# Optimization experiments

Measured on AMD Instinct MI355X. Metric: run time of the kernel, lower is better.

Reference implementation:

```python
import jax, jax.numpy as jnp
import numpy as np

WS = 16            # window size (patch grid)
NP = WS * WS       # 256 patch tokens
N = NP + 1         # +1 CLS
H = 16             # heads
LN_EPS = 1e-5


def _rel_pos_index():
    ch, cw = np.meshgrid(np.arange(WS), np.arange(WS), indexing='ij')
    flat = np.stack([ch.reshape(-1), cw.reshape(-1)])            # [2, NP]
    rel = flat[:, :, None] - flat[:, None, :]                    # [2, NP, NP]
    rel = rel.transpose(1, 2, 0).astype(np.int64)                # [NP, NP, 2]
    rel[:, :, 0] += WS - 1
    rel[:, :, 1] += WS - 1
    rel[:, :, 0] *= 2 * WS - 1
    nrd = (2 * WS - 1) * (2 * WS - 1) + 3                        # 964
    idx = np.zeros((N, N), dtype=np.int64)
    idx[1:, 1:] = rel.sum(-1)
    idx[0, 0:] = nrd - 3
    idx[0:, 0] = nrd - 2
    idx[0, 0] = nrd - 1
    return idx

REL_IDX = _rel_pos_index()


def layernorm(x, g, b):
    mu = x.mean(-1, keepdims=True)
    var = x.var(-1, keepdims=True)
    return (x - mu) * jax.lax.rsqrt(var + LN_EPS) * g + b


def rotate_half(t):
    t1, t2 = t[..., ::2], t[..., 1::2]
    return jnp.stack([-t2, t1], axis=-1).reshape(t.shape)


def apply_rope(t, cos, sin):
    # t: [B, H, NP, hd]; cos/sin: [NP, hd]
    return t * cos + rotate_half(t) * sin


def setup_inputs() -> dict:
    key = jax.random.key(0)
    ks = jax.random.split(key, 20)
    D, Hd = 1024, 4096
    s = lambda d: 1.0 / np.sqrt(d)
    return {
        'x': jax.random.normal(ks[0], (64, N, D), jnp.float32),
        'rope_cos': jnp.cos(jnp.arange(NP)[:, None] * jnp.exp(-jnp.arange(64) / 16.0)[None, :]),
        'rope_sin': jnp.sin(jnp.arange(NP)[:, None] * jnp.exp(-jnp.arange(64) / 16.0)[None, :]),
        'q_w': jax.random.normal(ks[1], (D, D)) * s(D),
        'q_b': jnp.zeros((D,)),
        'k_w': jax.random.normal(ks[2], (D, D)) * s(D),
        'v_w': jax.random.normal(ks[3], (D, D)) * s(D),
        'v_b': jnp.zeros((D,)),
        'rel_bias_table': jax.random.normal(ks[4], (964, H)) * 0.02,
        'inner_ln_g': jnp.ones((D,)), 'inner_ln_b': jnp.zeros((D,)),
        'proj_w': jax.random.normal(ks[5], (D, D)) * s(D),
        'proj_b': jnp.zeros((D,)),
        'norm1_g': jnp.ones((D,)), 'norm1_b': jnp.zeros((D,)),
        'norm2_g': jnp.ones((D,)), 'norm2_b': jnp.zeros((D,)),
        'w1_w': jax.random.normal(ks[6], (Hd, D)) * s(D),
        'w1_b': jnp.zeros((Hd,)),
        'w2_w': jax.random.normal(ks[7], (Hd, D)) * s(D),
        'w2_b': jnp.zeros((Hd,)),
        'ffn_ln_g': jnp.ones((Hd,)), 'ffn_ln_b': jnp.zeros((Hd,)),
        'w3_w': jax.random.normal(ks[8], (D, Hd)) * s(Hd),
        'w3_b': jnp.zeros((D,)),
    }


def reference(x, rope_cos, rope_sin, q_w, q_b, k_w, v_w, v_b, rel_bias_table,
              inner_ln_g, inner_ln_b, proj_w, proj_b, norm1_g, norm1_b,
              norm2_g, norm2_b, w1_w, w1_b, w2_w, w2_b, ffn_ln_g, ffn_ln_b,
              w3_w, w3_b):
    B, Ntok, D = x.shape
    hd = D // H
    scale = hd ** -0.5

    # ---- attention branch (pre-norm, subln path) ----
    xn = layernorm(x, norm1_g, norm1_b)
    q = (xn @ q_w.T + q_b).reshape(B, Ntok, H, hd).transpose(0, 2, 1, 3)
    k = (xn @ k_w.T).reshape(B, Ntok, H, hd).transpose(0, 2, 1, 3)
    v = (xn @ v_w.T + v_b).reshape(B, Ntok, H, hd).transpose(0, 2, 1, 3)

    # RoPE on all tokens except CLS
    q = jnp.concatenate([q[:, :, :1], apply_rope(q[:, :, 1:], rope_cos, rope_sin)], axis=2)
    k = jnp.concatenate([k[:, :, :1], apply_rope(k[:, :, 1:], rope_cos, rope_sin)], axis=2)

    attn = jnp.einsum('bhqd,bhkd->bhqk', q * scale, k)
    # relative position bias: [N, N, H] -> [H, N, N]
    rel_bias = rel_bias_table[REL_IDX.reshape(-1)].reshape(Ntok, Ntok, H).transpose(2, 0, 1)
    attn = attn + rel_bias[None]
    attn = jax.nn.softmax(attn, axis=-1)

    out = jnp.einsum('bhqk,bhkd->bqhd', attn, v).reshape(B, Ntok, D)
    out = layernorm(out, inner_ln_g, inner_ln_b)     # inner_attn_ln (subln)
    out = out @ proj_w.T + proj_b
    x = x + out

    # ---- SwiGLU MLP branch ----
    xn2 = layernorm(x, norm2_g, norm2_b)
    x1 = xn2 @ w1_w.T + w1_b
    x2 = xn2 @ w2_w.T + w2_b
    hidden = jax.nn.silu(x1) * x2
    hidden = layernorm(hidden, ffn_ln_g, ffn_ln_b)   # ffn_ln (subln)
    x = x + (hidden @ w3_w.T + w3_b)
    return x
```

## Files before the change

### kernel.cpp

```cpp
#include <hip/hip_runtime.h>
#include <stdint.h>

typedef __bf16 bf16;
typedef __attribute__((ext_vector_type(8))) __bf16 bf16x8;
typedef __attribute__((ext_vector_type(4))) float floatx4;

__device__ inline float bflo(uint32_t u){ union{uint32_t v; float f;} t; t.v = u << 16; return t.f; }
__device__ inline float bfhi(uint32_t u){ union{uint32_t v; float f;} t; t.v = u & 0xffff0000u; return t.f; }
__device__ inline uint32_t pack2(float a, float b){ union{ bf16 h[2]; uint32_t u; } t; t.h[0]=(bf16)a; t.h[1]=(bf16)b; return t.u; }

__device__ inline void load4(const bf16* p, float* x){
  uint2 u = *(const uint2*)p; x[0]=bflo(u.x); x[1]=bfhi(u.x); x[2]=bflo(u.y); x[3]=bfhi(u.y);
}
__device__ inline void load4(const float* p, float* x){
  float4 u = *(const float4*)p; x[0]=u.x; x[1]=u.y; x[2]=u.z; x[3]=u.w;
}

__device__ inline void gload16(const void* g, void* l){
  __builtin_amdgcn_global_load_lds((const __attribute__((address_space(1))) uint32_t*)g,
                                   (__attribute__((address_space(3))) uint32_t*)l, 16, 0, 0);
}

__global__ __launch_bounds__(256) void cvt_kernel(const float* __restrict__ in, bf16* __restrict__ out, int n8)
{
  int i = blockIdx.x * 256 + threadIdx.x;
  if (i >= n8) return;
  const float* p = in + (size_t)i * 8;
  float4 a = *(const float4*)p;
  float4 b = *(const float4*)(p + 4);
  union{ uint4 q; bf16 h[8]; } pk;
  pk.h[0]=(bf16)a.x; pk.h[1]=(bf16)a.y; pk.h[2]=(bf16)a.z; pk.h[3]=(bf16)a.w;
  pk.h[4]=(bf16)b.x; pk.h[5]=(bf16)b.y; pk.h[6]=(bf16)b.z; pk.h[7]=(bf16)b.w;
  *(uint4*)(out + (size_t)i*8) = pk.q;
}

template<int W, typename TIN>
__global__ __launch_bounds__(256) void ln_kernel(const TIN* in, const float* __restrict__ g,
                                                 const float* __restrict__ bb, bf16* out, int M)
{
  constexpr int E = W / 256;
  int row = blockIdx.x; if (row >= M) return;
  int tid = threadIdx.x;
  const TIN* rp = in + (size_t)row * W + tid * E;
  float x[E];
  #pragma unroll
  for (int j = 0; j < E; j += 4) load4(rp + j, &x[j]);
  float s = 0.f, ss = 0.f;
  #pragma unroll
  for (int e = 0; e < E; e++){ s += x[e]; ss += x[e]*x[e]; }
  #pragma unroll
  for (int k = 32; k >= 1; k >>= 1){ s += __shfl_xor(s, k, 64); ss += __shfl_xor(ss, k, 64); }
  __shared__ float rs_[4], rq_[4];
  if ((tid & 63) == 0){ rs_[tid >> 6] = s; rq_[tid >> 6] = ss; }
  __syncthreads();
  s = rs_[0]+rs_[1]+rs_[2]+rs_[3]; ss = rq_[0]+rq_[1]+rq_[2]+rq_[3];
  float mean = s * (1.0f / W);
  float var  = ss * (1.0f / W) - mean * mean;
  float rinv = rsqrtf(var + 1e-5f);
  bf16* op = out + (size_t)row * W + tid * E;
  const float* gp = g + tid * E;
  const float* bp = bb + tid * E;
  #pragma unroll
  for (int j = 0; j < E; j += 4){
    float gv[4], bv[4];
    load4(gp + j, gv); load4(bp + j, bv);
    float y0 = (x[j]  -mean)*rinv*gv[0] + bv[0];
    float y1 = (x[j+1]-mean)*rinv*gv[1] + bv[1];
    float y2 = (x[j+2]-mean)*rinv*gv[2] + bv[2];
    float y3 = (x[j+3]-mean)*rinv*gv[3] + bv[3];
    uint2 o; o.x = pack2(y0, y1); o.y = pack2(y2, y3);
    *(uint2*)(op + j) = o;
  }
}

template<typename TE, typename TC>
__global__ __launch_bounds__(256) void gemm_bt(const bf16* __restrict__ A, const bf16* __restrict__ Bw,
                                               const float* __restrict__ bias, const TE* extra,
                                               TC* C, int M, int N, int K, int mode)
{
  __shared__ __align__(16) bf16 As[128*32];
  __shared__ __align__(16) bf16 Bs[128*32];
  int tid = threadIdx.x;
  int lane = tid & 63, wave = tid >> 6;
  int l16 = lane & 15, quad = lane >> 4;
  int wm = wave >> 1, wn = wave & 1;
  int m0 = blockIdx.y * 128, n0 = blockIdx.x * 128;
  floatx4 acc[4][4];
  #pragma unroll
  for (int i = 0; i < 4; i++)
    #pragma unroll
    for (int j = 0; j < 4; j++) acc[i][j] = (floatx4){0.f,0.f,0.f,0.f};
  int nk = K >> 5;

  int rowS = tid >> 2;
  int colS = (tid & 3) * 8;
  int ra0 = min(m0 + rowS,      M-1);
  int ra1 = min(m0 + 64 + rowS, M-1);
  int rb0 = min(n0 + rowS,      N-1);
  int rb1 = min(n0 + 64 + rowS, N-1);
  const bf16* pa0 = A  + (size_t)ra0 * K + colS;
  const bf16* pa1 = A  + (size_t)ra1 * K + colS;
  const bf16* pb0 = Bw + (size_t)rb0 * K + colS;
  const bf16* pb1 = Bw + (size_t)rb1 * K + colS;
  bf16* la0 = &As[tid*8];        bf16* la1 = &As[2048 + tid*8];
  bf16* lb0 = &Bs[tid*8];        bf16* lb1 = &Bs[2048 + tid*8];
  auto stage = [&](int kt){
    int ko = kt * 32;
    gload16(pa0 + ko, la0);
    gload16(pa1 + ko, la1);
    gload16(pb0 + ko, lb0);
    gload16(pb1 + ko, lb1);
  };

  stage(0);
  int kt = 0;
  while (true){
    __syncthreads();
    bf16x8 af[4], bfv[4];
    #pragma unroll
    for (int i = 0; i < 4; i++) af[i]  = *(const bf16x8*)&As[(wm*64 + i*16 + l16)*32 + quad*8];
    #pragma unroll
    for (int j = 0; j < 4; j++) bfv[j] = *(const bf16x8*)&Bs[(wn*64 + j*16 + l16)*32 + quad*8];
    ++kt;
    bool more = kt < nk;
    if (more){
      __syncthreads();
      stage(kt);
    }
    #pragma unroll
    for (int i = 0; i < 4; i++)
      #pragma unroll
      for (int j = 0; j < 4; j++)
        acc[i][j] = __builtin_amdgcn_mfma_f32_16x16x32_bf16(af[i], bfv[j], acc[i][j], 0, 0, 0);
    if (!more) break;
  }

  #pragma unroll
  for (int i = 0; i < 4; i++){
    int gmb = m0 + wm*64 + i*16 + quad*4;
    #pragma unroll
    for (int j = 0; j < 4; j++){
      int gn = n0 + wn*64 + j*16 + l16;
      float bv = bias ? bias[gn] : 0.f;
      #pragma unroll
      for (int r = 0; r < 4; r++){
        int gm = gmb + r;
        if (gm < M){
          float v = acc[i][j][r] + bv;
          if (mode == 1) v += (float)extra[(size_t)gm * N + gn];
          else if (mode == 2){ float a = (float)extra[(size_t)gm * N + gn]; v *= a / (1.f + __expf(-a)); }
          C[(size_t)gm * N + gn] = (TC)v;
        }
      }
    }
  }
}

__global__ __launch_bounds__(256) void rope_kernel(bf16* __restrict__ q, bf16* __restrict__ k,
                                                   const float* __restrict__ cs, const float* __restrict__ sn)
{
  uint32_t i = blockIdx.x * 256u + threadIdx.x;
  int d0 = (int)(i & 511) * 2;
  int tok = (int)((i >> 9) & 255);
  int b = (int)(i >> 17);
  int j = d0 & 63;
  float c0 = cs[tok*64 + j], c1 = cs[tok*64 + j + 1];
  float s0 = sn[tok*64 + j], s1 = sn[tok*64 + j + 1];
  size_t off = ((size_t)(b*257 + tok + 1)) * 1024 + d0;
  uint32_t uq = *(const uint32_t*)(q + off);
  float x0 = bflo(uq), x1 = bfhi(uq);
  *(uint32_t*)(q + off) = pack2(x0*c0 - x1*s0, x1*c1 + x0*s1);
  uint32_t uk = *(const uint32_t*)(k + off);
  float y0 = bflo(uk), y1 = bfhi(uk);
  *(uint32_t*)(k + off) = pack2(y0*c0 - y1*s0, y1*c1 + y0*s1);
}

__global__ __launch_bounds__(256) void attn_kernel(const bf16* __restrict__ Q, const bf16* __restrict__ Kg,
                                                   const bf16* __restrict__ Vg, const float* __restrict__ tab,
                                                   bf16* __restrict__ AO)
{
  __shared__ __align__(16) bf16 Kc[144*64];
  __shared__ __align__(16) bf16 Vt[64*160];
  __shared__ __align__(16) float S[16*160];
  __shared__ __align__(16) bf16 P[16*160];
  __shared__ float mrow[16], lrow[16], arow[16];
  int id = blockIdx.x;
  int qt = id % 17; int rest = id / 17;
  int h = rest & 15; int b = rest >> 4;
  int tid = threadIdx.x; int wave = tid >> 6; int lane = tid & 63;
  int l16 = lane & 15, quad = lane >> 4;
  size_t base = ((size_t)b * 257) * 1024 + h * 64;
  int q0 = qt * 16;
  int tokA = min(q0 + l16, 256);
  const bf16* qp = Q + base + (size_t)tokA * 1024;
  bf16x8 a0 = *(const bf16x8*)(qp + quad*8);
  bf16x8 a1 = *(const bf16x8*)(qp + 32 + quad*8);
  floatx4 o = (floatx4){0.f,0.f,0.f,0.f};
  if (tid < 16){ mrow[tid] = -1e30f; lrow[tid] = 0.f; }
  for (int ch = 0; ch < 2; ch++){
    int t0 = ch * 144;
    __syncthreads();
    for (int i = tid; i < 144*8; i += 256){
      int row = i >> 3, c8 = (i & 7) * 8;
      int tok = t0 + row;
      uint4 u = make_uint4(0,0,0,0);
      if (tok <= 256) u = *(const uint4*)(Kg + base + (size_t)tok*1024 + c8);
      *(uint4*)&Kc[row*64 + c8] = u;
    }
    for (int i = tid; i < 160*8; i += 256){
      int trow = i >> 3, c8 = (i & 7) * 8;
      int tok = t0 + trow;
      uint4 u = make_uint4(0,0,0,0);
      if (trow < 144 && tok <= 256) u = *(const uint4*)(Vg + base + (size_t)tok*1024 + c8);
      union { uint4 q4; bf16 h8[8]; } tmp; tmp.q4 = u;
      #pragma unroll
      for (int jj = 0; jj < 8; jj++) Vt[(c8 + jj)*160 + trow] = tmp.h8[jj];
    }
    __syncthreads();
    for (int nt = wave; nt < 9; nt += 4){
      int kr = nt*16 + l16;
      bf16x8 b0 = *(const bf16x8*)&Kc[kr*64 + quad*8];
      bf16x8 b1 = *(const bf16x8*)&Kc[kr*64 + 32 + quad*8];
      floatx4 c = (floatx4){0.f,0.f,0.f,0.f};
      c = __builtin_amdgcn_mfma_f32_16x16x32_bf16(a0, b0, c, 0, 0, 0);
      c = __builtin_amdgcn_mfma_f32_16x16x32_bf16(a1, b1, c, 0, 0, 0);
      #pragma unroll
      for (int r = 0; r < 4; r++) S[(quad*4 + r)*160 + nt*16 + l16] = c[r];
    }
    __syncthreads();
    {
      int r = tid >> 4, li = tid & 15;
      int qg = q0 + r; bool vrow = qg <= 256;
      float vals[10]; float mc = -1e30f;
      #pragma unroll
      for (int jj = 0; jj < 10; jj++){
        int c = li + 16*jj; int kg = t0 + c;
        float sv = -1e30f;
        if (vrow && c < 144 && kg <= 256){
          int idx;
          if (qg == 0 && kg == 0) idx = 963;
          else if (qg == 0) idx = 961;
          else if (kg == 0) idx = 962;
          else { int p = qg - 1, pk = kg - 1;
                 idx = ((p >> 4) - (pk >> 4) + 15) * 31 + ((p & 15) - (pk & 15) + 15); }
          sv = S[r*160 + c] * 0.125f + tab[idx*16 + h];
        }
        vals[jj] = sv; mc = fmaxf(mc, sv);
      }
      #pragma unroll
      for (int k = 8; k >= 1; k >>= 1) mc = fmaxf(mc, __shfl_xor(mc, k, 16));
      float mold = mrow[r];
      float mnew = fmaxf(mold, mc);
      float alpha = __expf(mold - mnew);
      float sum = 0.f;
      #pragma unroll
      for (int jj = 0; jj < 10; jj++){
        float p = (vals[jj] > -1e29f) ? __expf(vals[jj] - mnew) : 0.f;
        sum += p;
        P[r*160 + li + 16*jj] = (bf16)p;
      }
      #pragma unroll
      for (int k = 8; k >= 1; k >>= 1) sum += __shfl_xor(sum, k, 16);
      if (li == 0){ mrow[r] = mnew; lrow[r] = lrow[r]*alpha + sum; arow[r] = alpha; }
    }
    __syncthreads();
    #pragma unroll
    for (int r2 = 0; r2 < 4; r2++) o[r2] *= arow[quad*4 + r2];
    #pragma unroll
    for (int ks = 0; ks < 5; ks++){
      bf16x8 pa = *(const bf16x8*)&P[l16*160 + ks*32 + quad*8];
      bf16x8 vb = *(const bf16x8*)&Vt[(wave*16 + l16)*160 + ks*32 + quad*8];
      o = __builtin_amdgcn_mfma_f32_16x16x32_bf16(pa, vb, o, 0, 0, 0);
    }
  }
  #pragma unroll
  for (int r2 = 0; r2 < 4; r2++){
    int qr = q0 + quad*4 + r2;
    if (qr <= 256){
      float inv = 1.0f / lrow[quad*4 + r2];
      AO[base + (size_t)qr*1024 + wave*16 + l16] = (bf16)(o[r2] * inv);
    }
  }
}

extern "C" void kernel_launch(void* const* d_in, const int* in_sizes, int n_in,
                              void* d_out, int out_size, void* d_ws, size_t ws_size,
                              hipStream_t stream)
{
  (void)in_sizes; (void)n_in; (void)out_size; (void)ws_size;
  const float* x    = (const float*)d_in[0];
  const float* rc   = (const float*)d_in[1];
  const float* rsn  = (const float*)d_in[2];
  const float* q_w  = (const float*)d_in[3];
  const float* q_b  = (const float*)d_in[4];
  const float* k_w  = (const float*)d_in[5];
  const float* v_w  = (const float*)d_in[6];
  const float* v_b  = (const float*)d_in[7];
  const float* tab  = (const float*)d_in[8];
  const float* ig   = (const float*)d_in[9];
  const float* ib   = (const float*)d_in[10];
  const float* pw   = (const float*)d_in[11];
  const float* pb   = (const float*)d_in[12];
  const float* n1g  = (const float*)d_in[13];
  const float* n1b  = (const float*)d_in[14];
  const float* n2g  = (const float*)d_in[15];
  const float* n2b  = (const float*)d_in[16];
  const float* w1w  = (const float*)d_in[17];
  const float* w1b  = (const float*)d_in[18];
  const float* w2w  = (const float*)d_in[19];
  const float* w2b  = (const float*)d_in[20];
  const float* fg   = (const float*)d_in[21];
  const float* fb   = (const float*)d_in[22];
  const float* w3w  = (const float*)d_in[23];
  const float* w3b  = (const float*)d_in[24];

  const int M = 64 * 257;
  const int D = 1024, HD = 4096;
  char* ws = (char*)d_ws;
  const size_t CHB = (size_t)M * D * 2;
  bf16* B0 = (bf16*)(ws);
  bf16* B1 = (bf16*)(ws + CHB);
  bf16* B2 = (bf16*)(ws + 2*CHB);
  bf16* B3 = (bf16*)(ws + 3*CHB);
  bf16* WQ = (bf16*)(ws + 4*CHB);
  bf16* WK = WQ + (size_t)D*D;
  bf16* WV = WK + (size_t)D*D;
  bf16* WP = WV + (size_t)D*D;
  bf16* W1 = WP + (size_t)D*D;
  bf16* W2 = W1 + (size_t)HD*D;
  bf16* W3 = W2 + (size_t)HD*D;
  bf16* XN  = B0;
  bf16* Qb  = B1;
  bf16* Kbf = B2;
  bf16* Vbf = B3;
  bf16* AO  = B0;
  bf16* AOL = B1;
  bf16* X1  = B2;
  bf16* XN2 = B3;
  bf16* HS  = B0;
  float* OUT = (float*)d_out;

  dim3 blk(256);
  dim3 g1(D/128, (M + 127)/128);

  const int n8_D = D*D/8;
  const int n8_H = HD*D/8;
  cvt_kernel<<<dim3(n8_D/256), blk, 0, stream>>>(q_w, WQ, n8_D);
  cvt_kernel<<<dim3(n8_D/256), blk, 0, stream>>>(k_w, WK, n8_D);
  cvt_kernel<<<dim3(n8_D/256), blk, 0, stream>>>(v_w, WV, n8_D);
  cvt_kernel<<<dim3(n8_D/256), blk, 0, stream>>>(pw,  WP, n8_D);
  cvt_kernel<<<dim3(n8_H/256), blk, 0, stream>>>(w1w, W1, n8_H);
  cvt_kernel<<<dim3(n8_H/256), blk, 0, stream>>>(w2w, W2, n8_H);
  cvt_kernel<<<dim3(n8_H/256), blk, 0, stream>>>(w3w, W3, n8_H);

  ln_kernel<1024, float><<<dim3(M), blk, 0, stream>>>(x, n1g, n1b, XN, M);
  gemm_bt<bf16, bf16><<<g1, blk, 0, stream>>>(XN, WQ, q_b, (const bf16*)nullptr, Qb, M, D, D, 0);
  gemm_bt<bf16, bf16><<<g1, blk, 0, stream>>>(XN, WK, nullptr, (const bf16*)nullptr, Kbf, M, D, D, 0);
  gemm_bt<bf16, bf16><<<g1, blk, 0, stream>>>(XN, WV, v_b, (const bf16*)nullptr, Vbf, M, D, D, 0);
  rope_kernel<<<dim3(64*256*512/256), blk, 0, stream>>>(Qb, Kbf, rc, rsn);
  attn_kernel<<<dim3(64*16*17), blk, 0, stream>>>(Qb, Kbf, Vbf, tab, AO);
  ln_kernel<1024, bf16><<<dim3(M), blk, 0, stream>>>(AO, ig, ib, AOL, M);
  gemm_bt<float, bf16><<<g1, blk, 0, stream>>>(AOL, WP, pb, x, X1, M, D, D, 1);
  ln_kernel<1024, bf16><<<dim3(M), blk, 0, stream>>>(X1, n2g, n2b, XN2, M);

  const int MC = M / 2;
  dim3 g2(HD/128, (MC + 127)/128);
  dim3 g1c(D/128, (MC + 127)/128);
  for (int c = 0; c < 2; c++){
    const bf16* a2 = XN2 + (size_t)c * MC * D;
    const bf16* x1 = X1  + (size_t)c * MC * D;
    float*      oc = OUT + (size_t)c * MC * D;
    gemm_bt<bf16, bf16><<<g2, blk, 0, stream>>>(a2, W1, w1b, (const bf16*)nullptr, HS, MC, HD, D, 0);
    gemm_bt<bf16, bf16><<<g2, blk, 0, stream>>>(a2, W2, w2b, HS, HS, MC, HD, D, 2);
    ln_kernel<4096, bf16><<<dim3(MC), blk, 0, stream>>>(HS, fg, fb, HS, MC);
    gemm_bt<bf16, float><<<g1c, blk, 0, stream>>>(HS, W3, w3b, x1, oc, MC, D, HD, 1);
  }
}
```

Measured before the change: 1.866 ms.

## Fuse QKV projection into one GEMM and rewrite attention as per-head single-pass

Merges the Q, K and V projections into a single GEMM with N=3072 by relying on the contiguous WQ/WK/WV weights and a combined bias buffer, and folds the softmax scale into the Q weights and bias. Precomputes the relative-position bias as a padded bf16 table stored temporarily in the output buffer. Rewrites attention so one block handles a whole (batch, head) pair: K is loaded once into swizzled LDS and V is transposed into LDS, then each wave computes full-row softmax in registers and moves P to the PV MFMA operand layout through lane shuffles instead of LDS. This removes repeated K/V reloads across query tiles, the online-softmax rescaling, and several LDS round trips, at the cost of more registers per wave and fewer blocks in flight.

```diff
diff --git a/kernel.cpp b/kernel.cpp
--- a/kernel.cpp
+++ b/kernel.cpp
@@ -21,7 +21,8 @@
                                    (__attribute__((address_space(3))) uint32_t*)l, 16, 0, 0);
 }
 
-__global__ __launch_bounds__(256) void cvt_kernel(const float* __restrict__ in, bf16* __restrict__ out, int n8)
+__global__ __launch_bounds__(256) void cvt_kernel(const float* __restrict__ in, bf16* __restrict__ out,
+                                                  int n8, float scale)
 {
   int i = blockIdx.x * 256 + threadIdx.x;
   if (i >= n8) return;
@@ -29,9 +30,42 @@
   float4 a = *(const float4*)p;
   float4 b = *(const float4*)(p + 4);
   union{ uint4 q; bf16 h[8]; } pk;
-  pk.h[0]=(bf16)a.x; pk.h[1]=(bf16)a.y; pk.h[2]=(bf16)a.z; pk.h[3]=(bf16)a.w;
-  pk.h[4]=(bf16)b.x; pk.h[5]=(bf16)b.y; pk.h[6]=(bf16)b.z; pk.h[7]=(bf16)b.w;
+  pk.h[0]=(bf16)(a.x*scale); pk.h[1]=(bf16)(a.y*scale); pk.h[2]=(bf16)(a.z*scale); pk.h[3]=(bf16)(a.w*scale);
+  pk.h[4]=(bf16)(b.x*scale); pk.h[5]=(bf16)(b.y*scale); pk.h[6]=(bf16)(b.z*scale); pk.h[7]=(bf16)(b.w*scale);
   *(uint4*)(out + (size_t)i*8) = pk.q;
+}
+
+__global__ __launch_bounds__(256) void qkvb_fill(const float* __restrict__ qb, const float* __restrict__ vb,
+                                                 float* __restrict__ out)
+{
+  int i = blockIdx.x * 256 + threadIdx.x;
+  float v = 0.f;
+  if (i < 1024) v = qb[i] * 0.125f;
+  else if (i >= 2048) v = vb[i - 2048];
+  out[i] = v;
+}
+
+__global__ __launch_bounds__(256) void bias_fill(const float* __restrict__ tab, bf16* __restrict__ biasB)
+{
+  int t = blockIdx.x * 256 + threadIdx.x;
+  if (t >= 16*272*272) return;
+  int kg = t % 272;
+  int rem = t / 272;
+  int qg = rem % 272;
+  int h = rem / 272;
+  float v;
+  if (kg > 256) v = -3e38f;
+  else {
+    int qq = min(qg, 256);
+    int idx;
+    if (qq == 0 && kg == 0) idx = 963;
+    else if (qq == 0) idx = 961;
+    else if (kg == 0) idx = 962;
+    else { int p = qq - 1, pk = kg - 1;
+           idx = ((p >> 4) - (pk >> 4) + 15) * 31 + ((p & 15) - (pk & 15) + 15); }
+    v = tab[idx*16 + h];
+  }
+  biasB[t] = (bf16)v;
 }
 
 template<int W, typename TIN>
@@ -91,7 +125,6 @@
     #pragma unroll
     for (int j = 0; j < 4; j++) acc[i][j] = (floatx4){0.f,0.f,0.f,0.f};
   int nk = K >> 5;
-
   int rowS = tid >> 2;
   int colS = (tid & 3) * 8;
   int ra0 = min(m0 + rowS,      M-1);
@@ -111,7 +144,6 @@
     gload16(pb0 + ko, lb0);
     gload16(pb1 + ko, lb1);
   };
-
   stage(0);
   int kt = 0;
   while (true){
@@ -134,7 +166,6 @@
         acc[i][j] = __builtin_amdgcn_mfma_f32_16x16x32_bf16(af[i], bfv[j], acc[i][j], 0, 0, 0);
     if (!more) break;
   }
-
   #pragma unroll
   for (int i = 0; i < 4; i++){
     int gmb = m0 + wm*64 + i*16 + quad*4;
@@ -156,7 +187,7 @@
   }
 }
 
-__global__ __launch_bounds__(256) void rope_kernel(bf16* __restrict__ q, bf16* __restrict__ k,
+__global__ __launch_bounds__(256) void rope_kernel(bf16* __restrict__ qkv,
                                                    const float* __restrict__ cs, const float* __restrict__ sn)
 {
   uint32_t i = blockIdx.x * 256u + threadIdx.x;
@@ -166,119 +197,136 @@
   int j = d0 & 63;
   float c0 = cs[tok*64 + j], c1 = cs[tok*64 + j + 1];
   float s0 = sn[tok*64 + j], s1 = sn[tok*64 + j + 1];
-  size_t off = ((size_t)(b*257 + tok + 1)) * 1024 + d0;
-  uint32_t uq = *(const uint32_t*)(q + off);
+  size_t off = ((size_t)(b*257 + tok + 1)) * 3072 + d0;
+  uint32_t uq = *(const uint32_t*)(qkv + off);
   float x0 = bflo(uq), x1 = bfhi(uq);
-  *(uint32_t*)(q + off) = pack2(x0*c0 - x1*s0, x1*c1 + x0*s1);
-  uint32_t uk = *(const uint32_t*)(k + off);
+  *(uint32_t*)(qkv + off) = pack2(x0*c0 - x1*s0, x1*c1 + x0*s1);
+  uint32_t uk = *(const uint32_t*)(qkv + off + 1024);
   float y0 = bflo(uk), y1 = bfhi(uk);
-  *(uint32_t*)(k + off) = pack2(y0*c0 - y1*s0, y1*c1 + y0*s1);
-}
-
-__global__ __launch_bounds__(256) void attn_kernel(const bf16* __restrict__ Q, const bf16* __restrict__ Kg,
-                                                   const bf16* __restrict__ Vg, const float* __restrict__ tab,
-                                                   bf16* __restrict__ AO)
-{
-  __shared__ __align__(16) bf16 Kc[144*64];
-  __shared__ __align__(16) bf16 Vt[64*160];
-  __shared__ __align__(16) float S[16*160];
-  __shared__ __align__(16) bf16 P[16*160];
-  __shared__ float mrow[16], lrow[16], arow[16];
+  *(uint32_t*)(qkv + off + 1024) = pack2(y0*c0 - y1*s0, y1*c1 + y0*s1);
+}
+
+__global__ __launch_bounds__(256, 2) void attn_kernel(const bf16* __restrict__ QKV,
+                                                      const bf16* __restrict__ biasB,
+                                                      bf16* __restrict__ AO)
+{
+  __shared__ __align__(16) bf16 Ks[272*64];
+  __shared__ __align__(16) bf16 Vt[64*296];
   int id = blockIdx.x;
-  int qt = id % 17; int rest = id / 17;
-  int h = rest & 15; int b = rest >> 4;
-  int tid = threadIdx.x; int wave = tid >> 6; int lane = tid & 63;
+  int h = id & 15, b = id >> 4;
+  int tid = threadIdx.x, lane = tid & 63, wave = tid >> 6;
   int l16 = lane & 15, quad = lane >> 4;
-  size_t base = ((size_t)b * 257) * 1024 + h * 64;
-  int q0 = qt * 16;
-  int tokA = min(q0 + l16, 256);
-  const bf16* qp = Q + base + (size_t)tokA * 1024;
-  bf16x8 a0 = *(const bf16x8*)(qp + quad*8);
-  bf16x8 a1 = *(const bf16x8*)(qp + 32 + quad*8);
-  floatx4 o = (floatx4){0.f,0.f,0.f,0.f};
-  if (tid < 16){ mrow[tid] = -1e30f; lrow[tid] = 0.f; }
-  for (int ch = 0; ch < 2; ch++){
-    int t0 = ch * 144;
-    __syncthreads();
-    for (int i = tid; i < 144*8; i += 256){
-      int row = i >> 3, c8 = (i & 7) * 8;
-      int tok = t0 + row;
-      uint4 u = make_uint4(0,0,0,0);
-      if (tok <= 256) u = *(const uint4*)(Kg + base + (size_t)tok*1024 + c8);
-      *(uint4*)&Kc[row*64 + c8] = u;
-    }
-    for (int i = tid; i < 160*8; i += 256){
-      int trow = i >> 3, c8 = (i & 7) * 8;
-      int tok = t0 + trow;
-      uint4 u = make_uint4(0,0,0,0);
-      if (trow < 144 && tok <= 256) u = *(const uint4*)(Vg + base + (size_t)tok*1024 + c8);
-      union { uint4 q4; bf16 h8[8]; } tmp; tmp.q4 = u;
+  size_t baseQ = (size_t)(b*257) * 3072 + h*64;
+  const bf16* Kg = QKV + baseQ + 1024;
+  const bf16* Vg = QKV + baseQ + 2048;
+  size_t aoBase = (size_t)(b*257) * 1024 + h*64;
+
+  for (int i = tid; i < 272*8; i += 256){
+    int row = i >> 3, seg = i & 7;
+    int tok = min(row, 256);
+    gload16(Kg + (size_t)tok*3072 + ((seg ^ (row & 7)) * 8), &Ks[i*8]);
+  }
+  for (int i = tid; i < 144*8; i += 256){
+    int tp = (i % 144) * 2, dseg = i / 144;
+    uint4 u0 = make_uint4(0,0,0,0), u1 = make_uint4(0,0,0,0);
+    if (tp     <= 256) u0 = *(const uint4*)(Vg + (size_t)tp*3072 + dseg*8);
+    if (tp + 1 <= 256) u1 = *(const uint4*)(Vg + (size_t)(tp+1)*3072 + dseg*8);
+    union { uint4 q4; bf16 h8[8]; } va, vb2; va.q4 = u0; vb2.q4 = u1;
+    #pragma unroll
+    for (int jj = 0; jj < 8; jj++){
+      union { uint32_t u; bf16 hh[2]; } w; w.hh[0] = va.h8[jj]; w.hh[1] = vb2.h8[jj];
+      *(uint32_t*)&Vt[(dseg*8 + jj)*296 + tp] = w.u;
+    }
+  }
+  __syncthreads();
+
+  int srcA = l16 + 16*((2*quad)     & 3);
+  int srcB = l16 + 16*((2*quad + 1) & 3);
+
+  for (int qt = wave; qt < 17; qt += 4){
+    int q0 = qt * 16;
+    int qrow = min(q0 + l16, 256);
+    const bf16* qp = QKV + baseQ + (size_t)qrow*3072;
+    bf16x8 qb0 = *(const bf16x8*)(qp + quad*8);
+    bf16x8 qb1 = *(const bf16x8*)(qp + 32 + quad*8);
+
+    floatx4 S[17];
+    #pragma unroll
+    for (int nt = 0; nt < 17; nt++){
+      int row = nt*16 + l16;
+      bf16x8 ka0 = *(const bf16x8*)&Ks[row*64 + ((quad     ^ (l16 & 7)) * 8)];
+      bf16x8 ka1 = *(const bf16x8*)&Ks[row*64 + (((4+quad) ^ (l16 & 7)) * 8)];
+      floatx4 c = (floatx4){0.f,0.f,0.f,0.f};
+      c = __builtin_amdgcn_mfma_f32_16x16x32_bf16(ka0, qb0, c, 0, 0, 0);
+      c = __builtin_amdgcn_mfma_f32_16x16x32_bf16(ka1, qb1, c, 0, 0, 0);
+      S[nt] = c;
+    }
+
+    const bf16* bp = biasB + ((size_t)(h*272) + (q0 + l16)) * 272;
+    float m = -3e38f;
+    #pragma unroll
+    for (int nt = 0; nt < 17; nt++){
+      uint2 bu = *(const uint2*)(bp + nt*16 + quad*4);
+      S[nt][0] += bflo(bu.x); S[nt][1] += bfhi(bu.x);
+      S[nt][2] += bflo(bu.y); S[nt][3] += bfhi(bu.y);
+      m = fmaxf(m, fmaxf(fmaxf(S[nt][0], S[nt][1]), fmaxf(S[nt][2], S[nt][3])));
+    }
+    m = fmaxf(m, __shfl_xor(m, 16, 64));
+    m = fmaxf(m, __shfl_xor(m, 32, 64));
+
+    float lsum = 0.f;
+    uint32_t pklo[17], pkhi[17];
+    #pragma unroll
+    for (int nt = 0; nt < 17; nt++){
+      float p0 = __expf(S[nt][0] - m), p1 = __expf(S[nt][1] - m);
+      float p2 = __expf(S[nt][2] - m), p3 = __expf(S[nt][3] - m);
+      lsum += (p0 + p1) + (p2 + p3);
+      pklo[nt] = pack2(p0, p1); pkhi[nt] = pack2(p2, p3);
+    }
+    lsum += __shfl_xor(lsum, 16, 64);
+    lsum += __shfl_xor(lsum, 32, 64);
+
+    floatx4 o[4];
+    #pragma unroll
+    for (int dt = 0; dt < 4; dt++) o[dt] = (floatx4){0.f,0.f,0.f,0.f};
+    #pragma unroll
+    for (int ks = 0; ks < 9; ks++){
+      uint32_t t0[4], t1[4];
+      t0[0] = (uint32_t)__shfl((int)pklo[2*ks], srcA, 64);
+      t0[1] = (uint32_t)__shfl((int)pkhi[2*ks], srcA, 64);
+      t0[2] = (uint32_t)__shfl((int)pklo[2*ks], srcB, 64);
+      t0[3] = (uint32_t)__shfl((int)pkhi[2*ks], srcB, 64);
+      if (2*ks + 1 <= 16){
+        t1[0] = (uint32_t)__shfl((int)pklo[2*ks+1], srcA, 64);
+        t1[1] = (uint32_t)__shfl((int)pkhi[2*ks+1], srcA, 64);
+        t1[2] = (uint32_t)__shfl((int)pklo[2*ks+1], srcB, 64);
+        t1[3] = (uint32_t)__shfl((int)pkhi[2*ks+1], srcB, 64);
+      } else {
+        t1[0] = 0; t1[1] = 0; t1[2] = 0; t1[3] = 0;
+      }
+      union { uint32_t u[4]; bf16x8 v; } pa;
+      bool lowhalf = (quad < 2);
+      pa.u[0] = lowhalf ? t0[0] : t1[0];
+      pa.u[1] = lowhalf ? t0[1] : t1[1];
+      pa.u[2] = lowhalf ? t0[2] : t1[2];
+      pa.u[3] = lowhalf ? t0[3] : t1[3];
       #pragma unroll
-      for (int jj = 0; jj < 8; jj++) Vt[(c8 + jj)*160 + trow] = tmp.h8[jj];
-    }
-    __syncthreads();
-    for (int nt = wave; nt < 9; nt += 4){
-      int kr = nt*16 + l16;
-      bf16x8 b0 = *(const bf16x8*)&Kc[kr*64 + quad*8];
-      bf16x8 b1 = *(const bf16x8*)&Kc[kr*64 + 32 + quad*8];
-      floatx4 c = (floatx4){0.f,0.f,0.f,0.f};
-      c = __builtin_amdgcn_mfma_f32_16x16x32_bf16(a0, b0, c, 0, 0, 0);
-      c = __builtin_amdgcn_mfma_f32_16x16x32_bf16(a1, b1, c, 0, 0, 0);
-      #pragma unroll
-      for (int r = 0; r < 4; r++) S[(quad*4 + r)*160 + nt*16 + l16] = c[r];
-    }
-    __syncthreads();
-    {
-      int r = tid >> 4, li = tid & 15;
-      int qg = q0 + r; bool vrow = qg <= 256;
-      float vals[10]; float mc = -1e30f;
-      #pragma unroll
-      for (int jj = 0; jj < 10; jj++){
-        int c = li + 16*jj; int kg = t0 + c;
-        float sv = -1e30f;
-        if (vrow && c < 144 && kg <= 256){
-          int idx;
-          if (qg == 0 && kg == 0) idx = 963;
-          else if (qg == 0) idx = 961;
-          else if (kg == 0) idx = 962;
-          else { int p = qg - 1, pk = kg - 1;
-                 idx = ((p >> 4) - (pk >> 4) + 15) * 31 + ((p & 15) - (pk & 15) + 15); }
-          sv = S[r*160 + c] * 0.125f + tab[idx*16 + h];
-        }
-        vals[jj] = sv; mc = fmaxf(mc, sv);
+      for (int dt = 0; dt < 4; dt++){
+        bf16x8 vb = *(const bf16x8*)&Vt[(dt*16 + l16)*296 + ks*32 + quad*8];
+        o[dt] = __builtin_amdgcn_mfma_f32_16x16x32_bf16(pa.v, vb, o[dt], 0, 0, 0);
       }
-      #pragma unroll
-      for (int k = 8; k >= 1; k >>= 1) mc = fmaxf(mc, __shfl_xor(mc, k, 16));
-      float mold = mrow[r];
-      float mnew = fmaxf(mold, mc);
-      float alpha = __expf(mold - mnew);
-      float sum = 0.f;
-      #pragma unroll
-      for (int jj = 0; jj < 10; jj++){
-        float p = (vals[jj] > -1e29f) ? __expf(vals[jj] - mnew) : 0.f;
-        sum += p;
-        P[r*160 + li + 16*jj] = (bf16)p;
+    }
+
+    #pragma unroll
+    for (int r = 0; r < 4; r++){
+      int q = q0 + quad*4 + r;
+      float ls = __shfl(lsum, quad*4 + r, 64);
+      float rinv = 1.0f / ls;
+      if (q <= 256){
+        #pragma unroll
+        for (int dt = 0; dt < 4; dt++)
+          AO[aoBase + (size_t)q*1024 + dt*16 + l16] = (bf16)(o[dt][r] * rinv);
       }
-      #pragma unroll
-      for (int k = 8; k >= 1; k >>= 1) sum += __shfl_xor(sum, k, 16);
-      if (li == 0){ mrow[r] = mnew; lrow[r] = lrow[r]*alpha + sum; arow[r] = alpha; }
-    }
-    __syncthreads();
-    #pragma unroll
-    for (int r2 = 0; r2 < 4; r2++) o[r2] *= arow[quad*4 + r2];
-    #pragma unroll
-    for (int ks = 0; ks < 5; ks++){
-      bf16x8 pa = *(const bf16x8*)&P[l16*160 + ks*32 + quad*8];
-      bf16x8 vb = *(const bf16x8*)&Vt[(wave*16 + l16)*160 + ks*32 + quad*8];
-      o = __builtin_amdgcn_mfma_f32_16x16x32_bf16(pa, vb, o, 0, 0, 0);
-    }
-  }
-  #pragma unroll
-  for (int r2 = 0; r2 < 4; r2++){
-    int qr = q0 + quad*4 + r2;
-    if (qr <= 256){
-      float inv = 1.0f / lrow[quad*4 + r2];
-      AO[base + (size_t)qr*1024 + wave*16 + l16] = (bf16)(o[r2] * inv);
     }
   }
 }
@@ -329,36 +377,37 @@
   bf16* W1 = WP + (size_t)D*D;
   bf16* W2 = W1 + (size_t)HD*D;
   bf16* W3 = W2 + (size_t)HD*D;
+  float* QKVB = (float*)(W3 + (size_t)HD*D);
   bf16* XN  = B0;
-  bf16* Qb  = B1;
-  bf16* Kbf = B2;
-  bf16* Vbf = B3;
+  bf16* QKV = B1;
   bf16* AO  = B0;
   bf16* AOL = B1;
   bf16* X1  = B2;
   bf16* XN2 = B3;
   bf16* HS  = B0;
+  bf16* biasB = (bf16*)d_out;
   float* OUT = (float*)d_out;
 
   dim3 blk(256);
   dim3 g1(D/128, (M + 127)/128);
+  dim3 gqkv(3072/128, (M + 127)/128);
 
   const int n8_D = D*D/8;
   const int n8_H = HD*D/8;
-  cvt_kernel<<<dim3(n8_D/256), blk, 0, stream>>>(q_w, WQ, n8_D);
-  cvt_kernel<<<dim3(n8_D/256), blk, 0, stream>>>(k_w, WK, n8_D);
-  cvt_kernel<<<dim3(n8_D/256), blk, 0, stream>>>(v_w, WV, n8_D);
-  cvt_kernel<<<dim3(n8_D/256), blk, 0, stream>>>(pw,  WP, n8_D);
-  cvt_kernel<<<dim3(n8_H/256), blk, 0, stream>>>(w1w, W1, n8_H);
-  cvt_kernel<<<dim3(n8_H/256), blk, 0, stream>>>(w2w, W2, n8_H);
-  cvt_kernel<<<dim3(n8_H/256), blk, 0, stream>>>(w3w, W3, n8_H);
+  cvt_kernel<<<dim3(n8_D/256), blk, 0, stream>>>(q_w, WQ, n8_D, 0.125f);
+  cvt_kernel<<<dim3(n8_D/256), blk, 0, stream>>>(k_w, WK, n8_D, 1.f);
+  cvt_kernel<<<dim3(n8_D/256), blk, 0, stream>>>(v_w, WV, n8_D, 1.f);
+  cvt_kernel<<<dim3(n8_D/256), blk, 0, stream>>>(pw,  WP, n8_D, 1.f);
+  cvt_kernel<<<dim3(n8_H/256), blk, 0, stream>>>(w1w, W1, n8_H, 1.f);
+  cvt_kernel<<<dim3(n8_H/256), blk, 0, stream>>>(w2w, W2, n8_H, 1.f);
+  cvt_kernel<<<dim3(n8_H/256), blk, 0, stream>>>(w3w, W3, n8_H, 1.f);
+  qkvb_fill<<<dim3(12), blk, 0, stream>>>(q_b, v_b, QKVB);
+  bias_fill<<<dim3((16*272*272 + 255)/256), blk, 0, stream>>>(tab, biasB);
 
   ln_kernel<1024, float><<<dim3(M), blk, 0, stream>>>(x, n1g, n1b, XN, M);
-  gemm_bt<bf16, bf16><<<g1, blk, 0, stream>>>(XN, WQ, q_b, (const bf16*)nullptr, Qb, M, D, D, 0);
-  gemm_bt<bf16, bf16><<<g1, blk, 0, stream>>>(XN, WK, nullptr, (const bf16*)nullptr, Kbf, M, D, D, 0);
-  gemm_bt<bf16, bf16><<<g1, blk, 0, stream>>>(XN, WV, v_b, (const bf16*)nullptr, Vbf, M, D, D, 0);
-  rope_kernel<<<dim3(64*256*512/256), blk, 0, stream>>>(Qb, Kbf, rc, rsn);
-  attn_kernel<<<dim3(64*16*17), blk, 0, stream>>>(Qb, Kbf, Vbf, tab, AO);
+  gemm_bt<bf16, bf16><<<gqkv, blk, 0, stream>>>(XN, WQ, QKVB, (const bf16*)nullptr, QKV, M, 3072, D, 0);
+  rope_kernel<<<dim3(64*256*512/256), blk, 0, stream>>>(QKV, rc, rsn);
+  attn_kernel<<<dim3(64*16), blk, 0, stream>>>(QKV, biasB, AO);
   ln_kernel<1024, bf16><<<dim3(M), blk, 0, stream>>>(AO, ig, ib, AOL, M);
   gemm_bt<float, bf16><<<g1, blk, 0, stream>>>(AOL, WP, pb, x, X1, M, D, D, 1);
   ln_kernel<1024, bf16><<<dim3(M), blk, 0, stream>>>(X1, n2g, n2b, XN2, M);
```

New measurement: 1.658 ms. 11.2% less time.
